# Optimization experiments

Measured on AMD Instinct MI355X. Metric: run time of the kernel, lower is better.

## Reference

```python
import jax, jax.numpy as jnp
import numpy as np

H, D = 12, 768
DH = D // H  # 64

def setup_inputs() -> dict:
    key = jax.random.key(0)
    ks = jax.random.split(key, 9)
    s = 0.02
    x  = jax.random.normal(ks[0], (8, 1024, D), dtype=jnp.float32)
    Wq = jax.random.normal(ks[1], (H, D, DH), dtype=jnp.float32) * s
    Wk = jax.random.normal(ks[2], (H, D, DH), dtype=jnp.float32) * s
    Wv = jax.random.normal(ks[3], (H, D, DH), dtype=jnp.float32) * s
    bq = jax.random.normal(ks[4], (H, DH), dtype=jnp.float32) * s
    bk = jax.random.normal(ks[5], (H, DH), dtype=jnp.float32) * s
    bv = jax.random.normal(ks[6], (H, DH), dtype=jnp.float32) * s
    Wo = jax.random.normal(ks[7], (D, D), dtype=jnp.float32) * s
    bo = jax.random.normal(ks[8], (D,), dtype=jnp.float32) * s
    return {"x": x, "Wq": Wq, "Wk": Wk, "Wv": Wv, "bq": bq, "bk": bk, "bv": bv, "Wo": Wo, "bo": bo}

def reference(x, Wq, Wk, Wv, bq, bk, bv, Wo, bo):
    # x: [B,S,D]; per-head projections batched over heads: [B,H,S,DH]
    q = jnp.einsum('bsd,hde->bhse', x, Wq) + bq[None, :, None, :]
    k = jnp.einsum('bsd,hde->bhse', x, Wk) + bk[None, :, None, :]
    v = jnp.einsum('bsd,hde->bhse', x, Wv) + bv[None, :, None, :]
    scores = jnp.einsum('bhse,bhte->bhst', q, k) / jnp.sqrt(jnp.float32(DH))
    probs = jax.nn.softmax(scores, axis=-1)  # dropout is identity (p=0 / eval)
    ctx = jnp.einsum('bhst,bhte->bhse', probs, v)  # [B,H,S,DH]
    B, _, S, _ = ctx.shape
    # concat heads along feature dim (head order matches torch cat order)
    ctx = jnp.transpose(ctx, (0, 2, 1, 3)).reshape(B, S, H * DH)
    out = jnp.einsum('bsd,de->bse', ctx, Wo) + bo
    return out
```

## Files before the change

### kernel.cpp

```cpp
#include <hip/hip_runtime.h>
#include <math.h>


constexpr int NB  = 8;
constexpr int SEQ = 1024;
constexpr int NH  = 12;
constexpr int DM  = 768;
constexpr int DHD = 64;
constexpr int MROWS = NB * SEQ;
constexpr int NQKV  = 3 * NH * DHD;

typedef __attribute__((ext_vector_type(8))) short short8;
typedef __attribute__((ext_vector_type(4))) float f32x4;

#define MFMA16(a,b,c) __builtin_amdgcn_mfma_f32_16x16x32_bf16((a),(b),(c),0,0,0)

#if __has_builtin(__builtin_amdgcn_exp2f)
#define EXP2(x) __builtin_amdgcn_exp2f(x)
#else
#define EXP2(x) exp2f(x)
#endif

__device__ __forceinline__ unsigned short f2bf(float f) {
    unsigned u = __float_as_uint(f);
    return (unsigned short)((u + 0x7fffu + ((u >> 16) & 1u)) >> 16);
}
__device__ __forceinline__ unsigned short f2bf_fast(float f) {
    return (unsigned short)((__float_as_uint(f) + 0x8000u) >> 16);
}

__device__ __forceinline__ void gl_lds16(const unsigned short* g, unsigned short* l) {
    __builtin_amdgcn_global_load_lds(
        (const __attribute__((address_space(1))) void*)g,
        (__attribute__((address_space(3))) void*)l, 16, 0, 0);
}

__device__ __forceinline__ void stageA(unsigned short* lds, const unsigned short* gbase,
                                       int i, int ln, int ldg) {
    int r    = i * 16 + (ln >> 2);
    int cpos = ln & 3;
    int cdat = (cpos - (r >> 1)) & 3;
    gl_lds16(gbase + (size_t)r * ldg + cdat * 8, lds + i * 512);
}
__device__ __forceinline__ short8 ldA(const unsigned short* buf, int row, int quad) {
    int c = (quad + (row >> 1)) & 3;
    return *(const short8*)&buf[row * 32 + c * 8];
}

__device__ __forceinline__ void stageK(unsigned short* lds, const unsigned short* gbase,
                                       int i, int ln, int ldg) {
    int r    = i * 8 + (ln >> 3);
    int cpos = ln & 7;
    int cdat = (cpos - r) & 7;
    gl_lds16(gbase + (size_t)r * ldg + cdat * 8, lds + i * 512);
}
__device__ __forceinline__ short8 ldK(const unsigned short* buf, int row, int chunk) {
    int c = (chunk + row) & 7;
    return *(const short8*)&buf[row * 64 + c * 8];
}

__global__ __launch_bounds__(256) void prep_k(
    const float* __restrict__ x,
    const float* __restrict__ Wq, const float* __restrict__ Wk,
    const float* __restrict__ Wv, const float* __restrict__ Wo,
    unsigned short* __restrict__ xb, unsigned short* __restrict__ wt,
    unsigned short* __restrict__ wot) {
    __shared__ float tb[64][65];
    const int blk = blockIdx.x, tid = threadIdx.x;
    if (blk < 6144) {
        const int i = blk * 256 + tid;
        float4 v = ((const float4*)x)[i];
        ushort4 o;
        o.x = f2bf(v.x); o.y = f2bf(v.y); o.z = f2bf(v.z); o.w = f2bf(v.w);
        ((ushort4*)xb)[i] = o;
        return;
    }
    const int t = blk - 6144;
    const int job = t / 144, lb = t % 144;
    const float* W;
    unsigned short* dst;
    int C, r0, c0;
    if (job < 3) {
        const float* Ws = (job == 0) ? Wq : (job == 1 ? Wk : Wv);
        const int h = lb / 12, rb = lb % 12;
        W = Ws + (size_t)h * (DM * DHD);
        dst = wt + (size_t)(job * 12 + h) * (DM * DHD);
        C = DHD; r0 = rb * 64; c0 = 0;
    } else {
        W = Wo; dst = wot; C = DM;
        r0 = (lb / 12) * 64; c0 = (lb % 12) * 64;
    }
    const int rr = tid >> 2, cc = (tid & 3) * 16;
#pragma unroll
    for (int j = 0; j < 16; j += 4) {
        float4 v = *(const float4*)&W[(size_t)(r0 + rr) * C + c0 + cc + j];
        tb[rr][cc + j + 0] = v.x;
        tb[rr][cc + j + 1] = v.y;
        tb[rr][cc + j + 2] = v.z;
        tb[rr][cc + j + 3] = v.w;
    }
    __syncthreads();
#pragma unroll
    for (int j = 0; j < 16; ++j)
        dst[(size_t)(c0 + rr) * DM + r0 + cc + j] = f2bf(tb[cc + j][rr]);
}

__global__ __launch_bounds__(256, 3) void qkv_mfma_k(
    const unsigned short* __restrict__ xb, const unsigned short* __restrict__ wt,
    const float* __restrict__ bq, const float* __restrict__ bk, const float* __restrict__ bv,
    unsigned short* __restrict__ qb, unsigned short* __restrict__ kb,
    unsigned short* __restrict__ vT) {
    __shared__ unsigned short Ah[128 * 32], Bh[128 * 32];

    const int tid = threadIdx.x;
    const int wv = tid >> 6, ln = tid & 63, quad = ln >> 4, lnid = ln & 15;
    const int wvm = wv >> 1, wvn = wv & 1;
    const int row0 = blockIdx.x * 128, col0 = blockIdx.y * 128;

    f32x4 acc[4][4];
#pragma unroll
    for (int i = 0; i < 4; ++i)
#pragma unroll
        for (int j = 0; j < 4; ++j) acc[i][j] = (f32x4){0.f, 0.f, 0.f, 0.f};

    const unsigned short* Ahg = xb + (size_t)row0 * DM;
    const unsigned short* Bhg = wt + (size_t)col0 * DM;

    for (int kc = 0; kc < DM; kc += 32) {
        __syncthreads();
        stageA(Ah, Ahg + kc, wv * 2, ln, DM);
        stageA(Ah, Ahg + kc, wv * 2 + 1, ln, DM);
        stageA(Bh, Bhg + kc, wv * 2, ln, DM);
        stageA(Bh, Bhg + kc, wv * 2 + 1, ln, DM);
        __syncthreads();

        short8 a[4], b[4];
#pragma unroll
        for (int i = 0; i < 4; ++i) a[i] = ldA(Ah, wvm * 64 + i * 16 + lnid, quad);
#pragma unroll
        for (int j = 0; j < 4; ++j) b[j] = ldA(Bh, wvn * 64 + j * 16 + lnid, quad);
#pragma unroll
        for (int i = 0; i < 4; ++i)
#pragma unroll
            for (int j = 0; j < 4; ++j) acc[i][j] = MFMA16(a[i], b[j], acc[i][j]);
    }

    const int sel = (col0 >= 2 * DM) ? 2 : (col0 >= DM ? 1 : 0);
    const float scale = (sel == 0) ? 0.18033688011112042f : 1.0f;
    const float* bias = (sel == 0) ? bq : (sel == 1 ? bk : bv);
    unsigned short* oh = (sel == 0) ? qb : kb;

#pragma unroll
    for (int i = 0; i < 4; ++i) {
#pragma unroll
        for (int j = 0; j < 4; ++j) {
            const int col = col0 + wvn * 64 + j * 16 + lnid;
            const int he = col - sel * DM;
            const int hh2 = he >> 6, ee = he & 63;
            const float bs = bias[he];
            if (sel < 2) {
#pragma unroll
                for (int r = 0; r < 4; ++r) {
                    const int srow = row0 + wvm * 64 + i * 16 + quad * 4 + r;
                    const int bb = srow >> 10, ss = srow & (SEQ - 1);
                    oh[((size_t)(bb * NH + hh2) * SEQ + ss) * DHD + ee] =
                        f2bf((acc[i][j][r] + bs) * scale);
                }
            } else {
                const int srow = row0 + wvm * 64 + i * 16 + quad * 4;
                const int bb = srow >> 10, ss = srow & (SEQ - 1);
                ushort4 pk;
                pk.x = f2bf(acc[i][j][0] + bs);
                pk.y = f2bf(acc[i][j][1] + bs);
                pk.z = f2bf(acc[i][j][2] + bs);
                pk.w = f2bf(acc[i][j][3] + bs);
                *(ushort4*)&vT[((size_t)(bb * NH + hh2) * DHD + ee) * SEQ + ss] = pk;
            }
        }
    }
}

__global__ __launch_bounds__(256, 3) void attn_mfma_k(
    const unsigned short* __restrict__ qb, const unsigned short* __restrict__ kb,
    const unsigned short* __restrict__ vT, unsigned short* __restrict__ ctb) {
    __shared__ unsigned short ksh[2][64 * 64], vsm[2][64 * 64];
    __shared__ unsigned short ps[128 * 72];

    const int tid = threadIdx.x;
    const int wv = tid >> 6, ln = tid & 63, quad = ln >> 4, lnid = ln & 15;
    const int bhid = blockIdx.x % 96, qt = blockIdx.x / 96;
    const int b = bhid / NH, h = bhid % NH;
    const int q0 = qt * 128;
    const unsigned short* qhb = qb + (size_t)bhid * (SEQ * DHD);
    const unsigned short* khb = kb + (size_t)bhid * (SEQ * DHD);
    const unsigned short* vTb = vT + (size_t)bhid * (DHD * SEQ);

    short8 qf[2][2];
#pragma unroll
    for (int mt = 0; mt < 2; ++mt) {
        const int srow = q0 + wv * 32 + mt * 16 + lnid;
#pragma unroll
        for (int ks_ = 0; ks_ < 2; ++ks_)
            qf[mt][ks_] = *(const short8*)(qhb + (size_t)srow * DHD + ks_ * 32 + quad * 8);
    }

    f32x4 ctx[2][4];
#pragma unroll
    for (int i = 0; i < 2; ++i)
#pragma unroll
        for (int j = 0; j < 4; ++j) ctx[i][j] = (f32x4){0.f, 0.f, 0.f, 0.f};
    float lsum[2][4] = {};

    stageK(ksh[0], khb, wv * 2, ln, DHD);
    stageK(ksh[0], khb, wv * 2 + 1, ln, DHD);
    stageK(vsm[0], vTb, wv * 2, ln, SEQ);
    stageK(vsm[0], vTb, wv * 2 + 1, ln, SEQ);

    for (int kt = 0; kt < SEQ / 64; ++kt) {
        const int cur = kt & 1;
        __syncthreads();
        if (kt + 1 < SEQ / 64) {
            const unsigned short* kn = khb + (kt + 1) * 64 * DHD;
            const unsigned short* vn = vTb + (kt + 1) * 64;
            stageK(ksh[cur ^ 1], kn, wv * 2, ln, DHD);
            stageK(ksh[cur ^ 1], kn, wv * 2 + 1, ln, DHD);
            stageK(vsm[cur ^ 1], vn, wv * 2, ln, SEQ);
            stageK(vsm[cur ^ 1], vn, wv * 2 + 1, ln, SEQ);
        }

        f32x4 sc[2][4];
#pragma unroll
        for (int i = 0; i < 2; ++i)
#pragma unroll
            for (int j = 0; j < 4; ++j) sc[i][j] = (f32x4){0.f, 0.f, 0.f, 0.f};
#pragma unroll
        for (int ks_ = 0; ks_ < 2; ++ks_) {
#pragma unroll
            for (int nt = 0; nt < 4; ++nt) {
                short8 k_h = ldK(ksh[cur], nt * 16 + lnid, ks_ * 4 + quad);
                sc[0][nt] = MFMA16(qf[0][ks_], k_h, sc[0][nt]);
                sc[1][nt] = MFMA16(qf[1][ks_], k_h, sc[1][nt]);
            }
        }

#pragma unroll
        for (int mt = 0; mt < 2; ++mt)
#pragma unroll
            for (int nt = 0; nt < 4; ++nt)
#pragma unroll
                for (int r = 0; r < 4; ++r) {
                    float p = EXP2(sc[mt][nt][r]);
                    lsum[mt][r] += p;
                    ps[(wv * 32 + mt * 16 + quad * 4 + r) * 72 + nt * 16 + lnid] =
                        f2bf_fast(p);
                }

#pragma unroll
        for (int kvs = 0; kvs < 2; ++kvs) {
            short8 pa0 = *(const short8*)&ps[(wv * 32 + lnid) * 72 + kvs * 32 + quad * 8];
            short8 pa1 = *(const short8*)&ps[(wv * 32 + 16 + lnid) * 72 + kvs * 32 + quad * 8];
#pragma unroll
            for (int nt = 0; nt < 4; ++nt) {
                short8 v8 = ldK(vsm[cur], nt * 16 + lnid, kvs * 4 + quad);
                ctx[0][nt] = MFMA16(pa0, v8, ctx[0][nt]);
                ctx[1][nt] = MFMA16(pa1, v8, ctx[1][nt]);
            }
        }
    }

#pragma unroll
    for (int mt = 0; mt < 2; ++mt) {
#pragma unroll
        for (int r = 0; r < 4; ++r) {
            float s = lsum[mt][r];
#pragma unroll
            for (int off = 1; off < 16; off <<= 1) s += __shfl_xor(s, off, 64);
            const float inv = 1.0f / s;
            const int srow = b * SEQ + q0 + wv * 32 + mt * 16 + quad * 4 + r;
#pragma unroll
            for (int nt = 0; nt < 4; ++nt)
                ctb[(size_t)srow * DM + h * DHD + nt * 16 + lnid] =
                    f2bf(ctx[mt][nt][r] * inv);
        }
    }
}

__global__ __launch_bounds__(256, 3) void out_mfma_k(
    const unsigned short* __restrict__ ctb, const unsigned short* __restrict__ wot,
    const float* __restrict__ bo, float* __restrict__ out) {
    __shared__ unsigned short Ah[128 * 32], Bh[128 * 32];

    const int tid = threadIdx.x;
    const int wv = tid >> 6, ln = tid & 63, quad = ln >> 4, lnid = ln & 15;
    const int wvm = wv >> 1, wvn = wv & 1;
    const int row0 = blockIdx.x * 128, col0 = blockIdx.y * 128;

    f32x4 acc[4][4];
#pragma unroll
    for (int i = 0; i < 4; ++i)
#pragma unroll
        for (int j = 0; j < 4; ++j) acc[i][j] = (f32x4){0.f, 0.f, 0.f, 0.f};

    const unsigned short* Ahg = ctb + (size_t)row0 * DM;
    const unsigned short* Bhg = wot + (size_t)col0 * DM;

    for (int kc = 0; kc < DM; kc += 32) {
        __syncthreads();
        stageA(Ah, Ahg + kc, wv * 2, ln, DM);
        stageA(Ah, Ahg + kc, wv * 2 + 1, ln, DM);
        stageA(Bh, Bhg + kc, wv * 2, ln, DM);
        stageA(Bh, Bhg + kc, wv * 2 + 1, ln, DM);
        __syncthreads();

        short8 a[4], b[4];
#pragma unroll
        for (int i = 0; i < 4; ++i) a[i] = ldA(Ah, wvm * 64 + i * 16 + lnid, quad);
#pragma unroll
        for (int j = 0; j < 4; ++j) b[j] = ldA(Bh, wvn * 64 + j * 16 + lnid, quad);
#pragma unroll
        for (int i = 0; i < 4; ++i)
#pragma unroll
            for (int j = 0; j < 4; ++j) acc[i][j] = MFMA16(a[i], b[j], acc[i][j]);
    }

#pragma unroll
    for (int i = 0; i < 4; ++i)
#pragma unroll
        for (int j = 0; j < 4; ++j) {
            const int col = col0 + wvn * 64 + j * 16 + lnid;
            const float bs = bo[col];
#pragma unroll
            for (int r = 0; r < 4; ++r) {
                const int srow = row0 + wvm * 64 + i * 16 + quad * 4 + r;
                out[(size_t)srow * DM + col] = acc[i][j][r] + bs;
            }
        }
}

extern "C" void kernel_launch(void* const* d_in, const int* in_sizes, int n_in,
                              void* d_out, int out_size, void* d_ws, size_t ws_size,
                              hipStream_t stream) {
    const float* x  = (const float*)d_in[0];
    const float* Wq = (const float*)d_in[1];
    const float* Wk = (const float*)d_in[2];
    const float* Wv = (const float*)d_in[3];
    const float* bq = (const float*)d_in[4];
    const float* bk = (const float*)d_in[5];
    const float* bv = (const float*)d_in[6];
    const float* Wo = (const float*)d_in[7];
    const float* bo = (const float*)d_in[8];
    float* out = (float*)d_out;

    char* w = (char*)d_ws;
    const size_t elsX = (size_t)MROWS * DM;
    const size_t elsQ = (size_t)NB * NH * SEQ * DHD;
    unsigned short* xb  = (unsigned short*)w;
    unsigned short* ctb = xb;
    size_t off = elsX * 2;
    unsigned short* wt  = (unsigned short*)(w + off); off += (size_t)NQKV * DM * 2;
    unsigned short* wot = (unsigned short*)(w + off); off += (size_t)DM * DM * 2;
    unsigned short* qbp = (unsigned short*)(w + off); off += elsQ * 2;
    unsigned short* kbp = (unsigned short*)(w + off); off += elsQ * 2;
    unsigned short* vTp = (unsigned short*)(w + off); off += elsQ * 2;

    prep_k<<<dim3(6144 + 576), 256, 0, stream>>>(x, Wq, Wk, Wv, Wo, xb, wt, wot);
    qkv_mfma_k<<<dim3(MROWS / 128, NQKV / 128), 256, 0, stream>>>(
        xb, wt, bq, bk, bv, qbp, kbp, vTp);
    attn_mfma_k<<<dim3(768), 256, 0, stream>>>(qbp, kbp, vTp, ctb);
    out_mfma_k<<<dim3(MROWS / 128, DM / 128), 256, 0, stream>>>(ctb, wot, bo, out);
}
```

Before: 203.5 us.

## Swap MFMA operand order for vectorized epilogues and widen GEMM K-step to 64

```diff
diff --git a/kernel.cpp b/kernel.cpp
--- a/kernel.cpp
+++ b/kernel.cpp
@@ -33,18 +33,6 @@
     __builtin_amdgcn_global_load_lds(
         (const __attribute__((address_space(1))) void*)g,
         (__attribute__((address_space(3))) void*)l, 16, 0, 0);
-}
-
-__device__ __forceinline__ void stageA(unsigned short* lds, const unsigned short* gbase,
-                                       int i, int ln, int ldg) {
-    int r    = i * 16 + (ln >> 2);
-    int cpos = ln & 3;
-    int cdat = (cpos - (r >> 1)) & 3;
-    gl_lds16(gbase + (size_t)r * ldg + cdat * 8, lds + i * 512);
-}
-__device__ __forceinline__ short8 ldA(const unsigned short* buf, int row, int quad) {
-    int c = (quad + (row >> 1)) & 3;
-    return *(const short8*)&buf[row * 32 + c * 8];
 }
 
 __device__ __forceinline__ void stageK(unsigned short* lds, const unsigned short* gbase,
@@ -110,12 +98,13 @@
     const float* __restrict__ bq, const float* __restrict__ bk, const float* __restrict__ bv,
     unsigned short* __restrict__ qb, unsigned short* __restrict__ kb,
     unsigned short* __restrict__ vT) {
-    __shared__ unsigned short Ah[128 * 32], Bh[128 * 32];
+    __shared__ unsigned short Ah[128 * 64], Bh[128 * 64];
 
     const int tid = threadIdx.x;
     const int wv = tid >> 6, ln = tid & 63, quad = ln >> 4, lnid = ln & 15;
     const int wvm = wv >> 1, wvn = wv & 1;
     const int row0 = blockIdx.x * 128, col0 = blockIdx.y * 128;
+    const int sel = (col0 >= 2 * DM) ? 2 : (col0 >= DM ? 1 : 0);
 
     f32x4 acc[4][4];
 #pragma unroll
@@ -125,48 +114,89 @@
 
     const unsigned short* Ahg = xb + (size_t)row0 * DM;
     const unsigned short* Bhg = wt + (size_t)col0 * DM;
-
-    for (int kc = 0; kc < DM; kc += 32) {
-        __syncthreads();
-        stageA(Ah, Ahg + kc, wv * 2, ln, DM);
-        stageA(Ah, Ahg + kc, wv * 2 + 1, ln, DM);
-        stageA(Bh, Bhg + kc, wv * 2, ln, DM);
-        stageA(Bh, Bhg + kc, wv * 2 + 1, ln, DM);
-        __syncthreads();
-
-        short8 a[4], b[4];
-#pragma unroll
-        for (int i = 0; i < 4; ++i) a[i] = ldA(Ah, wvm * 64 + i * 16 + lnid, quad);
-#pragma unroll
-        for (int j = 0; j < 4; ++j) b[j] = ldA(Bh, wvn * 64 + j * 16 + lnid, quad);
-#pragma unroll
-        for (int i = 0; i < 4; ++i)
-#pragma unroll
-            for (int j = 0; j < 4; ++j) acc[i][j] = MFMA16(a[i], b[j], acc[i][j]);
-    }
-
-    const int sel = (col0 >= 2 * DM) ? 2 : (col0 >= DM ? 1 : 0);
-    const float scale = (sel == 0) ? 0.18033688011112042f : 1.0f;
-    const float* bias = (sel == 0) ? bq : (sel == 1 ? bk : bv);
-    unsigned short* oh = (sel == 0) ? qb : kb;
-
-#pragma unroll
-    for (int i = 0; i < 4; ++i) {
-#pragma unroll
-        for (int j = 0; j < 4; ++j) {
-            const int col = col0 + wvn * 64 + j * 16 + lnid;
-            const int he = col - sel * DM;
+    constexpr int NIT = DM / 64;
+
+    if (sel < 2) {
+        for (int it = 0; it < NIT; ++it) {
+            const int kc = it * 64;
+            __syncthreads();
+#pragma unroll
+            for (int c = 0; c < 4; ++c) {
+                stageK(Ah, Ahg + kc, wv * 4 + c, ln, DM);
+                stageK(Bh, Bhg + kc, wv * 4 + c, ln, DM);
+            }
+            __syncthreads();
+#pragma unroll
+            for (int ks = 0; ks < 2; ++ks) {
+                short8 a[4], b[4];
+#pragma unroll
+                for (int i = 0; i < 4; ++i)
+                    a[i] = ldK(Ah, wvm * 64 + i * 16 + lnid, ks * 4 + quad);
+#pragma unroll
+                for (int j = 0; j < 4; ++j)
+                    b[j] = ldK(Bh, wvn * 64 + j * 16 + lnid, ks * 4 + quad);
+#pragma unroll
+                for (int j = 0; j < 4; ++j)
+#pragma unroll
+                    for (int i = 0; i < 4; ++i)
+                        acc[j][i] = MFMA16(b[j], a[i], acc[j][i]);
+            }
+        }
+        const float scale = (sel == 0) ? 0.18033688011112042f : 1.0f;
+        const float* bias = (sel == 0) ? bq : bk;
+        unsigned short* oh = (sel == 0) ? qb : kb;
+#pragma unroll
+        for (int et = 0; et < 4; ++et) {
+            const int e = col0 + wvn * 64 + et * 16 + quad * 4;
+            const int he = e - sel * DM;
             const int hh2 = he >> 6, ee = he & 63;
-            const float bs = bias[he];
-            if (sel < 2) {
-#pragma unroll
-                for (int r = 0; r < 4; ++r) {
-                    const int srow = row0 + wvm * 64 + i * 16 + quad * 4 + r;
-                    const int bb = srow >> 10, ss = srow & (SEQ - 1);
-                    oh[((size_t)(bb * NH + hh2) * SEQ + ss) * DHD + ee] =
-                        f2bf((acc[i][j][r] + bs) * scale);
-                }
-            } else {
+            float4 bs = *(const float4*)&bias[he];
+#pragma unroll
+            for (int st = 0; st < 4; ++st) {
+                const int srow = row0 + wvm * 64 + st * 16 + lnid;
+                const int bb = srow >> 10, ss = srow & (SEQ - 1);
+                ushort4 pk;
+                pk.x = f2bf((acc[et][st][0] + bs.x) * scale);
+                pk.y = f2bf((acc[et][st][1] + bs.y) * scale);
+                pk.z = f2bf((acc[et][st][2] + bs.z) * scale);
+                pk.w = f2bf((acc[et][st][3] + bs.w) * scale);
+                *(ushort4*)&oh[((size_t)(bb * NH + hh2) * SEQ + ss) * DHD + ee] = pk;
+            }
+        }
+    } else {
+        for (int it = 0; it < NIT; ++it) {
+            const int kc = it * 64;
+            __syncthreads();
+#pragma unroll
+            for (int c = 0; c < 4; ++c) {
+                stageK(Ah, Ahg + kc, wv * 4 + c, ln, DM);
+                stageK(Bh, Bhg + kc, wv * 4 + c, ln, DM);
+            }
+            __syncthreads();
+#pragma unroll
+            for (int ks = 0; ks < 2; ++ks) {
+                short8 a[4], b[4];
+#pragma unroll
+                for (int i = 0; i < 4; ++i)
+                    a[i] = ldK(Ah, wvm * 64 + i * 16 + lnid, ks * 4 + quad);
+#pragma unroll
+                for (int j = 0; j < 4; ++j)
+                    b[j] = ldK(Bh, wvn * 64 + j * 16 + lnid, ks * 4 + quad);
+#pragma unroll
+                for (int i = 0; i < 4; ++i)
+#pragma unroll
+                    for (int j = 0; j < 4; ++j)
+                        acc[i][j] = MFMA16(a[i], b[j], acc[i][j]);
+            }
+        }
+#pragma unroll
+        for (int i = 0; i < 4; ++i) {
+#pragma unroll
+            for (int j = 0; j < 4; ++j) {
+                const int col = col0 + wvn * 64 + j * 16 + lnid;
+                const int he = col - 2 * DM;
+                const int hh2 = he >> 6, ee = he & 63;
+                const float bs = bv[he];
                 const int srow = row0 + wvm * 64 + i * 16 + quad * 4;
                 const int bb = srow >> 10, ss = srow & (SEQ - 1);
                 ushort4 pk;
@@ -209,7 +239,7 @@
     for (int i = 0; i < 2; ++i)
 #pragma unroll
         for (int j = 0; j < 4; ++j) ctx[i][j] = (f32x4){0.f, 0.f, 0.f, 0.f};
-    float lsum[2][4] = {};
+    float lsum[2] = {0.f, 0.f};
 
     stageK(ksh[0], khb, wv * 2, ln, DHD);
     stageK(ksh[0], khb, wv * 2 + 1, ln, DHD);
@@ -238,49 +268,58 @@
 #pragma unroll
             for (int nt = 0; nt < 4; ++nt) {
                 short8 k_h = ldK(ksh[cur], nt * 16 + lnid, ks_ * 4 + quad);
-                sc[0][nt] = MFMA16(qf[0][ks_], k_h, sc[0][nt]);
-                sc[1][nt] = MFMA16(qf[1][ks_], k_h, sc[1][nt]);
-            }
-        }
-
-#pragma unroll
-        for (int mt = 0; mt < 2; ++mt)
-#pragma unroll
-            for (int nt = 0; nt < 4; ++nt)
-#pragma unroll
-                for (int r = 0; r < 4; ++r) {
-                    float p = EXP2(sc[mt][nt][r]);
-                    lsum[mt][r] += p;
-                    ps[(wv * 32 + mt * 16 + quad * 4 + r) * 72 + nt * 16 + lnid] =
-                        f2bf_fast(p);
-                }
+                sc[0][nt] = MFMA16(k_h, qf[0][ks_], sc[0][nt]);
+                sc[1][nt] = MFMA16(k_h, qf[1][ks_], sc[1][nt]);
+            }
+        }
+
+#pragma unroll
+        for (int mt = 0; mt < 2; ++mt) {
+            const int prow = wv * 32 + mt * 16 + lnid;
+#pragma unroll
+            for (int nt = 0; nt < 4; ++nt) {
+                float p0 = EXP2(sc[mt][nt][0]);
+                float p1 = EXP2(sc[mt][nt][1]);
+                float p2 = EXP2(sc[mt][nt][2]);
+                float p3 = EXP2(sc[mt][nt][3]);
+                lsum[mt] += (p0 + p1) + (p2 + p3);
+                ushort4 pw;
+                pw.x = f2bf_fast(p0);
+                pw.y = f2bf_fast(p1);
+                pw.z = f2bf_fast(p2);
+                pw.w = f2bf_fast(p3);
+                *(ushort4*)&ps[prow * 72 + nt * 16 + quad * 4] = pw;
+            }
+        }
 
 #pragma unroll
         for (int kvs = 0; kvs < 2; ++kvs) {
-            short8 pa0 = *(const short8*)&ps[(wv * 32 + lnid) * 72 + kvs * 32 + quad * 8];
-            short8 pa1 = *(const short8*)&ps[(wv * 32 + 16 + lnid) * 72 + kvs * 32 + quad * 8];
-#pragma unroll
-            for (int nt = 0; nt < 4; ++nt) {
-                short8 v8 = ldK(vsm[cur], nt * 16 + lnid, kvs * 4 + quad);
-                ctx[0][nt] = MFMA16(pa0, v8, ctx[0][nt]);
-                ctx[1][nt] = MFMA16(pa1, v8, ctx[1][nt]);
+            short8 pf0 = *(const short8*)&ps[(wv * 32 + lnid) * 72 + kvs * 32 + quad * 8];
+            short8 pf1 = *(const short8*)&ps[(wv * 32 + 16 + lnid) * 72 + kvs * 32 + quad * 8];
+#pragma unroll
+            for (int dt = 0; dt < 4; ++dt) {
+                short8 vf = ldK(vsm[cur], dt * 16 + lnid, kvs * 4 + quad);
+                ctx[0][dt] = MFMA16(vf, pf0, ctx[0][dt]);
+                ctx[1][dt] = MFMA16(vf, pf1, ctx[1][dt]);
             }
         }
     }
 
 #pragma unroll
     for (int mt = 0; mt < 2; ++mt) {
-#pragma unroll
-        for (int r = 0; r < 4; ++r) {
-            float s = lsum[mt][r];
-#pragma unroll
-            for (int off = 1; off < 16; off <<= 1) s += __shfl_xor(s, off, 64);
-            const float inv = 1.0f / s;
-            const int srow = b * SEQ + q0 + wv * 32 + mt * 16 + quad * 4 + r;
-#pragma unroll
-            for (int nt = 0; nt < 4; ++nt)
-                ctb[(size_t)srow * DM + h * DHD + nt * 16 + lnid] =
-                    f2bf(ctx[mt][nt][r] * inv);
+        float s = lsum[mt];
+        s += __shfl_xor(s, 16, 64);
+        s += __shfl_xor(s, 32, 64);
+        const float inv = 1.0f / s;
+        const int srow = b * SEQ + q0 + wv * 32 + mt * 16 + lnid;
+#pragma unroll
+        for (int dt = 0; dt < 4; ++dt) {
+            ushort4 pk;
+            pk.x = f2bf(ctx[mt][dt][0] * inv);
+            pk.y = f2bf(ctx[mt][dt][1] * inv);
+            pk.z = f2bf(ctx[mt][dt][2] * inv);
+            pk.w = f2bf(ctx[mt][dt][3] * inv);
+            *(ushort4*)&ctb[(size_t)srow * DM + h * DHD + dt * 16 + quad * 4] = pk;
         }
     }
 }
@@ -288,53 +327,63 @@
 __global__ __launch_bounds__(256, 3) void out_mfma_k(
     const unsigned short* __restrict__ ctb, const unsigned short* __restrict__ wot,
     const float* __restrict__ bo, float* __restrict__ out) {
-    __shared__ unsigned short Ah[128 * 32], Bh[128 * 32];
+    __shared__ unsigned short Ah[128 * 64], Bh[64 * 64];
 
     const int tid = threadIdx.x;
     const int wv = tid >> 6, ln = tid & 63, quad = ln >> 4, lnid = ln & 15;
     const int wvm = wv >> 1, wvn = wv & 1;
-    const int row0 = blockIdx.x * 128, col0 = blockIdx.y * 128;
-
-    f32x4 acc[4][4];
-#pragma unroll
-    for (int i = 0; i < 4; ++i)
-#pragma unroll
-        for (int j = 0; j < 4; ++j) acc[i][j] = (f32x4){0.f, 0.f, 0.f, 0.f};
+    const int row0 = blockIdx.x * 128, col0 = blockIdx.y * 64;
+
+    f32x4 acc[2][4];
+#pragma unroll
+    for (int j = 0; j < 2; ++j)
+#pragma unroll
+        for (int i = 0; i < 4; ++i) acc[j][i] = (f32x4){0.f, 0.f, 0.f, 0.f};
 
     const unsigned short* Ahg = ctb + (size_t)row0 * DM;
     const unsigned short* Bhg = wot + (size_t)col0 * DM;
 
-    for (int kc = 0; kc < DM; kc += 32) {
+    constexpr int NIT = DM / 64;
+    for (int it = 0; it < NIT; ++it) {
+        const int kc = it * 64;
         __syncthreads();
-        stageA(Ah, Ahg + kc, wv * 2, ln, DM);
-        stageA(Ah, Ahg + kc, wv * 2 + 1, ln, DM);
-        stageA(Bh, Bhg + kc, wv * 2, ln, DM);
-        stageA(Bh, Bhg + kc, wv * 2 + 1, ln, DM);
+#pragma unroll
+        for (int c = 0; c < 4; ++c) stageK(Ah, Ahg + kc, wv * 4 + c, ln, DM);
+#pragma unroll
+        for (int c = 0; c < 2; ++c) stageK(Bh, Bhg + kc, wv * 2 + c, ln, DM);
         __syncthreads();
-
-        short8 a[4], b[4];
-#pragma unroll
-        for (int i = 0; i < 4; ++i) a[i] = ldA(Ah, wvm * 64 + i * 16 + lnid, quad);
-#pragma unroll
-        for (int j = 0; j < 4; ++j) b[j] = ldA(Bh, wvn * 64 + j * 16 + lnid, quad);
-#pragma unroll
-        for (int i = 0; i < 4; ++i)
-#pragma unroll
-            for (int j = 0; j < 4; ++j) acc[i][j] = MFMA16(a[i], b[j], acc[i][j]);
-    }
-
-#pragma unroll
-    for (int i = 0; i < 4; ++i)
-#pragma unroll
-        for (int j = 0; j < 4; ++j) {
-            const int col = col0 + wvn * 64 + j * 16 + lnid;
-            const float bs = bo[col];
-#pragma unroll
-            for (int r = 0; r < 4; ++r) {
-                const int srow = row0 + wvm * 64 + i * 16 + quad * 4 + r;
-                out[(size_t)srow * DM + col] = acc[i][j][r] + bs;
-            }
-        }
+#pragma unroll
+        for (int ks = 0; ks < 2; ++ks) {
+            short8 a[4], b[2];
+#pragma unroll
+            for (int i = 0; i < 4; ++i)
+                a[i] = ldK(Ah, wvm * 64 + i * 16 + lnid, ks * 4 + quad);
+#pragma unroll
+            for (int j = 0; j < 2; ++j)
+                b[j] = ldK(Bh, wvn * 32 + j * 16 + lnid, ks * 4 + quad);
+#pragma unroll
+            for (int j = 0; j < 2; ++j)
+#pragma unroll
+                for (int i = 0; i < 4; ++i)
+                    acc[j][i] = MFMA16(b[j], a[i], acc[j][i]);
+        }
+    }
+
+#pragma unroll
+    for (int jt = 0; jt < 2; ++jt) {
+        const int colb = col0 + wvn * 32 + jt * 16 + quad * 4;
+        float4 bs = *(const float4*)&bo[colb];
+#pragma unroll
+        for (int it = 0; it < 4; ++it) {
+            const int srow = row0 + wvm * 64 + it * 16 + lnid;
+            float4 o;
+            o.x = acc[jt][it][0] + bs.x;
+            o.y = acc[jt][it][1] + bs.y;
+            o.z = acc[jt][it][2] + bs.z;
+            o.w = acc[jt][it][3] + bs.w;
+            *(float4*)&out[(size_t)srow * DM + colb] = o;
+        }
+    }
 }
 
 extern "C" void kernel_launch(void* const* d_in, const int* in_sizes, int n_in,
@@ -367,5 +416,5 @@
     qkv_mfma_k<<<dim3(MROWS / 128, NQKV / 128), 256, 0, stream>>>(
         xb, wt, bq, bk, bv, qbp, kbp, vTp);
     attn_mfma_k<<<dim3(768), 256, 0, stream>>>(qbp, kbp, vTp, ctb);
-    out_mfma_k<<<dim3(MROWS / 128, DM / 128), 256, 0, stream>>>(ctb, wot, bo, out);
-}
+    out_mfma_k<<<dim3(MROWS / 128, DM / 64), 256, 0, stream>>>(ctb, wot, bo, out);
+}
```

Measured after the change: 195.6 us. 1.04x faster.
